# Kernel tuning notes

Measured on AMD Instinct MI355X. Metric: run time of the kernel, lower is better.

## Reference

```python
import jax, jax.numpy as jnp
import numpy as np

DIM_Q = 512
DIM_K = 512
DIM_V = 512
NUM_HEADS = 8
TEMPERATURE = 0.1
LN_EPS = 1e-5


def setup_inputs() -> dict:
    key = jax.random.key(0)
    ks = jax.random.split(key, 12)
    B, n_q, n_k = 8, 1024, 1024
    s = 0.02
    return {
        "Q": jax.random.normal(ks[0], (B, n_q, DIM_Q), jnp.float32),
        "K": jax.random.normal(ks[1], (B, n_k, DIM_K), jnp.float32),
        "mask": jnp.ones((B, n_k), dtype=bool),
        "Wq": jax.random.normal(ks[2], (DIM_Q, DIM_V), jnp.float32) * s,
        "bq": jnp.zeros((DIM_V,), jnp.float32),
        "Wk": jax.random.normal(ks[3], (DIM_K, DIM_V), jnp.float32) * s,
        "bk": jnp.zeros((DIM_V,), jnp.float32),
        "Wv": jax.random.normal(ks[4], (DIM_K, DIM_V), jnp.float32) * s,
        "bv": jnp.zeros((DIM_V,), jnp.float32),
        "Wo": jax.random.normal(ks[5], (DIM_V, DIM_V), jnp.float32) * s,
        "bo": jnp.zeros((DIM_V,), jnp.float32),
        "gamma": jnp.ones((DIM_V,), jnp.float32),
        "beta": jnp.zeros((DIM_V,), jnp.float32),
    }


def _mab(Q, K, mask, Wq, bq, Wk, bk, Wv, bv, Wo, bo, gamma, beta):
    B, n_q, _ = Q.shape
    n_k = K.shape[1]
    H = NUM_HEADS
    d_head = DIM_V // H
    # projections, split heads: [B, H, n, d_head]
    Qh = (Q @ Wq + bq).reshape(B, n_q, H, d_head).transpose(0, 2, 1, 3)
    Kh = (K @ Wk + bk).reshape(B, n_k, H, d_head).transpose(0, 2, 1, 3)
    Vh = (K @ Wv + bv).reshape(B, n_k, H, d_head).transpose(0, 2, 1, 3)
    scale = 1.0 / (np.sqrt(d_head) * TEMPERATURE)
    A = jnp.einsum("bhqd,bhkd->bhqk", Qh, Kh) * scale
    A = jnp.where(mask[:, None, None, :], A, -jnp.inf)
    A = jax.nn.softmax(A, axis=-1)
    O = jnp.einsum("bhqk,bhkd->bhqd", A, Vh)
    O = O.transpose(0, 2, 1, 3).reshape(B, n_q, DIM_V)
    # fused output FFN + residual + LN
    O = O + jax.nn.relu(O @ Wo + bo)
    mu = jnp.mean(O, axis=-1, keepdims=True)
    var = jnp.var(O, axis=-1, keepdims=True)
    return (O - mu) * jax.lax.rsqrt(var + LN_EPS) * gamma + beta


def reference(Q, K, mask, Wq, bq, Wk, bk, Wv, bv, Wo, bo, gamma, beta):
    return _mab(Q, K, mask, Wq, bq, Wk, bk, Wv, bv, Wo, bo, gamma, beta)
```

## Files before the change

kernel.cpp:

```cpp
#include <hip/hip_runtime.h>

typedef __bf16 bf16;
typedef bf16 bf16x4 __attribute__((ext_vector_type(4)));
typedef bf16 bf16x8 __attribute__((ext_vector_type(8)));
typedef float floatx4 __attribute__((ext_vector_type(4)));

#define NB 8
#define NQ 1024
#define NK 1024
#define DIM 512
#define NH 8
#define DH 64

__device__ __forceinline__ void async16(const void* g, void* l) {
    __builtin_amdgcn_global_load_lds(
        (const __attribute__((address_space(1))) unsigned int*)(unsigned long long)(g),
        (__attribute__((address_space(3))) unsigned int*)(unsigned long long)(l),
        16, 0, 0);
}

__global__ __launch_bounds__(256) void prep_fused(
    const float* __restrict__ Q, const float* __restrict__ K,
    const float* __restrict__ Wq, const float* __restrict__ Wk,
    const float* __restrict__ Wv, const float* __restrict__ Wo,
    bf16* __restrict__ Qb, bf16* __restrict__ Kb, bf16* __restrict__ Wt)
{
    __shared__ bf16 Tl[64][68];
    const int bid = blockIdx.x;
    if (bid < 4096) {
        const int i = bid * 256 + threadIdx.x;
        float4 a = ((const float4*)Q)[i];
        float4 c = ((const float4*)K)[i];
        bf16x4 qa = {(bf16)a.x, (bf16)a.y, (bf16)a.z, (bf16)a.w};
        bf16x4 ka = {(bf16)c.x, (bf16)c.y, (bf16)c.z, (bf16)c.w};
        *(bf16x4*)(Qb + (size_t)i * 4) = qa;
        *(bf16x4*)(Kb + (size_t)i * 4) = ka;
    } else {
        const int bid2 = bid - 4096;
        const int w = bid2 >> 6;
        const int bx = bid2 & 7, by = (bid2 >> 3) & 7;
        const float* W = (w == 0) ? Wq : (w == 1) ? Wk : (w == 2) ? Wv : Wo;
        bf16* out = Wt + (size_t)w * DIM * DIM;
        const int k0 = bx * 64, n0 = by * 64;
        const int tx = threadIdx.x & 15, ty = threadIdx.x >> 4;
        for (int pass = 0; pass < 4; ++pass) {
            int k = ty + pass * 16;
            float4 v = *(const float4*)&W[(size_t)(k0 + k) * DIM + n0 + tx * 4];
            Tl[tx * 4 + 0][k] = (bf16)v.x;
            Tl[tx * 4 + 1][k] = (bf16)v.y;
            Tl[tx * 4 + 2][k] = (bf16)v.z;
            Tl[tx * 4 + 3][k] = (bf16)v.w;
        }
        __syncthreads();
        for (int pass = 0; pass < 4; ++pass) {
            int n = ty + pass * 16;
            bf16x4 ov = *(const bf16x4*)&Tl[n][tx * 4];
            *(bf16x4*)&out[(size_t)(n0 + n) * DIM + k0 + tx * 4] = ov;
        }
    }
}

__global__ __launch_bounds__(256) void proj_fused(
    const bf16* __restrict__ Qb, const bf16* __restrict__ Kb,
    const bf16* __restrict__ Wt,
    const float* __restrict__ bq, const float* __restrict__ bk,
    const float* __restrict__ bv,
    bf16* __restrict__ Qp, bf16* __restrict__ Kp, bf16* __restrict__ Vpt)
{
    __shared__ __attribute__((aligned(16))) bf16 sh[24576];
    const int t = threadIdx.x;
    const int wave = t >> 6, lane = t & 63, quad = lane >> 4, l16 = lane & 15;
    const int wr = wave >> 1, wc = wave & 1;
    const int bid = blockIdx.x;
    const bool isQ = bid < 512;
    const bf16* A; const bf16* W; int m0, n0;
    if (isQ) { A = Qb; W = Wt;             m0 = (bid & 63) * 128;  n0 = (bid >> 6) * 64; }
    else     { int b2 = bid - 512;
               A = Kb; W = Wt + 512 * DIM; m0 = (b2 & 63) * 128;   n0 = (b2 >> 6) * 64; }

    const int r1 = t >> 3, s1 = t & 7;
    const int p1 = s1 ^ (r1 & 7);
    const bf16* aSrc = A + (size_t)(m0 + r1) * DIM + p1 * 8;
    const bf16* wSrc = W + (size_t)(n0 + r1) * DIM + p1 * 8;

    floatx4 acc[4][2];
    for (int i = 0; i < 4; ++i)
        for (int j = 0; j < 2; ++j) acc[i][j] = (floatx4){0.f, 0.f, 0.f, 0.f};

    #pragma unroll
    for (int j = 0; j < 4; ++j)
        async16(aSrc + (size_t)j * 32 * DIM, sh + (t + j * 256) * 8);
    #pragma unroll
    for (int j = 0; j < 2; ++j)
        async16(wSrc + (size_t)j * 32 * DIM, sh + 16384 + (t + j * 256) * 8);

    for (int kt = 0; kt < 8; ++kt) {
        __syncthreads();
        const int cur = kt & 1;
        bf16* Acur = sh + cur * 8192;
        bf16* Bcur = sh + 16384 + cur * 4096;
        if (kt < 7) {
            bf16* Anxt = sh + (1 - cur) * 8192;
            bf16* Bnxt = sh + 16384 + (1 - cur) * 4096;
            const int ko = (kt + 1) * 64;
            #pragma unroll
            for (int j = 0; j < 4; ++j)
                async16(aSrc + ko + (size_t)j * 32 * DIM, Anxt + (t + j * 256) * 8);
            #pragma unroll
            for (int j = 0; j < 2; ++j)
                async16(wSrc + ko + (size_t)j * 32 * DIM, Bnxt + (t + j * 256) * 8);
        }
        #pragma unroll
        for (int ks = 0; ks < 2; ++ks) {
            bf16x8 af[4], bfr[2];
            #pragma unroll
            for (int mi = 0; mi < 4; ++mi) {
                const int row = wr * 64 + mi * 16 + l16;
                af[mi] = *(const bf16x8*)(Acur + row * 64 + (((ks * 4 + quad) ^ (row & 7)) << 3));
            }
            #pragma unroll
            for (int ni = 0; ni < 2; ++ni) {
                const int row = wc * 32 + ni * 16 + l16;
                bfr[ni] = *(const bf16x8*)(Bcur + row * 64 + (((ks * 4 + quad) ^ (row & 7)) << 3));
            }
            #pragma unroll
            for (int mi = 0; mi < 4; ++mi)
                #pragma unroll
                for (int ni = 0; ni < 2; ++ni)
                    acc[mi][ni] = __builtin_amdgcn_mfma_f32_16x16x32_bf16(
                        af[mi], bfr[ni], acc[mi][ni], 0, 0, 0);
        }
    }

    const bool isV = (!isQ) && (n0 >= 512);
    if (!isV) {
        bf16* out = isQ ? Qp : Kp;
        const float* bias = isQ ? bq : bk;
        const float qscale = isQ ? 1.8033688f : 1.0f;
        for (int ni = 0; ni < 2; ++ni) {
            const int n = n0 + wc * 32 + ni * 16 + l16;
            const float bb = bias[n];
            const int hd = n >> 6, d = n & 63;
            for (int mi = 0; mi < 4; ++mi) {
                for (int r = 0; r < 4; ++r) {
                    const int m = m0 + wr * 64 + mi * 16 + quad * 4 + r;
                    const int b = m >> 10, q = m & 1023;
                    out[((size_t)(b * 8 + hd) * 1024 + q) * 64 + d] =
                        (bf16)((acc[mi][ni][r] + bb) * qscale);
                }
            }
        }
    } else {
        __syncthreads();
        for (int ni = 0; ni < 2; ++ni) {
            const int n = wc * 32 + ni * 16 + l16;
            const float bb = bv[n0 + n - 512];
            for (int mi = 0; mi < 4; ++mi) {
                const int mb = wr * 64 + mi * 16 + quad * 4;
                const int slot = ((mb >> 3) ^ (n & 15));
                bf16x4 pk = {(bf16)(acc[mi][ni][0] + bb), (bf16)(acc[mi][ni][1] + bb),
                             (bf16)(acc[mi][ni][2] + bb), (bf16)(acc[mi][ni][3] + bb)};
                *(bf16x4*)(sh + n * 128 + slot * 8 + (mb & 7)) = pk;
            }
        }
        __syncthreads();
        const int n = t >> 2, hf = t & 3;
        const int nv = n0 + n - 512, hd = nv >> 6, d = nv & 63;
        const int b = m0 >> 10, qb = m0 & 1023;
        bf16* dst = Vpt + ((size_t)(b * 8 + hd) * 64 + d) * 1024 + qb;
        #pragma unroll
        for (int j = 0; j < 4; ++j) {
            const int ch = hf * 4 + j;
            const int slot = ch ^ (n & 15);
            bf16x8 v8 = *(const bf16x8*)(sh + n * 128 + slot * 8);
            *(bf16x8*)(dst + ch * 8) = v8;
        }
    }
}

__global__ __launch_bounds__(256) void attn_kernel(
    const bf16* __restrict__ Qp, const bf16* __restrict__ Kp,
    const bf16* __restrict__ Vpt, const int* __restrict__ mask,
    bf16* __restrict__ Oa)
{
    const int bh = blockIdx.x & 63, qblk = blockIdx.x >> 6;
    const int b = bh >> 3, hd = bh & 7;
    const int t = threadIdx.x;
    const int wave = t >> 6, lane = t & 63, quad = lane >> 4, l16 = lane & 15;

    __shared__ __attribute__((aligned(16))) bf16 Kt[2][64 * 64];
    __shared__ __attribute__((aligned(16))) bf16 Vt[2][64 * 64];
    __shared__ __attribute__((aligned(16))) bf16 Pl[4][16 * 64];

    const bf16* Qbase = Qp + ((size_t)bh * NQ + qblk * 64 + wave * 16) * DH;
    const bf16* Kbase = Kp + (size_t)bh * NK * DH;
    const bf16* Vbase = Vpt + (size_t)bh * DH * NK;
    const int* mrow = mask + b * NK;

    bf16x8 qf[2];
    #pragma unroll
    for (int hh = 0; hh < 2; ++hh)
        qf[hh] = *(const bf16x8*)(Qbase + (size_t)l16 * DH + hh * 32 + quad * 8);

    bf16x8 onesv;
    #pragma unroll
    for (int j = 0; j < 8; ++j) onesv[j] = (bf16)1.0f;

    floatx4 o[4];
    floatx4 osum = (floatx4){0.f, 0.f, 0.f, 0.f};
    #pragma unroll
    for (int i = 0; i < 4; ++i) o[i] = (floatx4){0.f, 0.f, 0.f, 0.f};

    const int r1 = t >> 3, s1 = t & 7;
    const int p1 = s1 ^ (r1 & 7);
    const bf16* kSrc = Kbase + r1 * 64 + p1 * 8;
    const bf16* vSrc = Vbase + (size_t)r1 * 1024 + p1 * 8;

    async16(kSrc, Kt[0] + t * 8);
    async16(kSrc + 32 * 64, Kt[0] + (t + 256) * 8);
    async16(vSrc, Vt[0] + t * 8);
    async16(vSrc + (size_t)32 * 1024, Vt[0] + (t + 256) * 8);

    for (int kt = 0; kt < NK / 64; ++kt) {
        __syncthreads();
        const int cur = kt & 1;
        if (kt < NK / 64 - 1) {
            const int nxt = 1 - cur;
            async16(kSrc + (kt + 1) * 4096, Kt[nxt] + t * 8);
            async16(kSrc + (kt + 1) * 4096 + 32 * 64, Kt[nxt] + (t + 256) * 8);
            async16(vSrc + (kt + 1) * 64, Vt[nxt] + t * 8);
            async16(vSrc + (kt + 1) * 64 + (size_t)32 * 1024, Vt[nxt] + (t + 256) * 8);
        }

        bf16x8 kb[4][2];
        #pragma unroll
        for (int sub = 0; sub < 4; ++sub) {
            const int rowk = sub * 16 + l16;
            kb[sub][0] = *(const bf16x8*)(Kt[cur] + rowk * 64 + ((quad ^ (rowk & 7)) << 3));
            kb[sub][1] = *(const bf16x8*)(Kt[cur] + rowk * 64 + (((quad + 4) ^ (rowk & 7)) << 3));
        }
        floatx4 sf[4];
        __builtin_amdgcn_s_setprio(1);
        #pragma unroll
        for (int sub = 0; sub < 4; ++sub) {
            floatx4 s = {0.f, 0.f, 0.f, 0.f};
            s = __builtin_amdgcn_mfma_f32_16x16x32_bf16(kb[sub][0], qf[0], s, 0, 0, 0);
            s = __builtin_amdgcn_mfma_f32_16x16x32_bf16(kb[sub][1], qf[1], s, 0, 0, 0);
            sf[sub] = s;
        }
        __builtin_amdgcn_s_setprio(0);

        const int mv = mrow[kt * 64 + lane];
        if (!__all(mv != 0)) {
            #pragma unroll
            for (int sub = 0; sub < 4; ++sub) {
                const int4 m4 = *(const int4*)&mrow[kt * 64 + sub * 16 + quad * 4];
                if (!m4.x) sf[sub][0] = -3.0e38f;
                if (!m4.y) sf[sub][1] = -3.0e38f;
                if (!m4.z) sf[sub][2] = -3.0e38f;
                if (!m4.w) sf[sub][3] = -3.0e38f;
            }
        }
        #pragma unroll
        for (int sub = 0; sub < 4; ++sub) {
            sf[sub][0] = __builtin_amdgcn_exp2f(sf[sub][0]);
            sf[sub][1] = __builtin_amdgcn_exp2f(sf[sub][1]);
            sf[sub][2] = __builtin_amdgcn_exp2f(sf[sub][2]);
            sf[sub][3] = __builtin_amdgcn_exp2f(sf[sub][3]);
        }
        #pragma unroll
        for (int sub = 0; sub < 4; ++sub) {
            bf16x4 pk = {(bf16)sf[sub][0], (bf16)sf[sub][1],
                         (bf16)sf[sub][2], (bf16)sf[sub][3]};
            const int slot = (sub * 2 + (quad >> 1)) ^ (l16 & 7);
            *(bf16x4*)&Pl[wave][l16 * 64 + slot * 8 + (quad & 1) * 4] = pk;
        }
        bf16x8 af[2];
        #pragma unroll
        for (int hh = 0; hh < 2; ++hh) {
            const int slot = (hh * 4 + quad) ^ (l16 & 7);
            af[hh] = *(const bf16x8*)&Pl[wave][l16 * 64 + slot * 8];
        }
        __builtin_amdgcn_s_setprio(1);
        osum = __builtin_amdgcn_mfma_f32_16x16x32_bf16(af[0], onesv, osum, 0, 0, 0);
        osum = __builtin_amdgcn_mfma_f32_16x16x32_bf16(af[1], onesv, osum, 0, 0, 0);
        #pragma unroll
        for (int dsub = 0; dsub < 4; ++dsub) {
            const int rowd = dsub * 16 + l16;
            bf16x8 v0 = *(const bf16x8*)(Vt[cur] + rowd * 64 + ((quad ^ (rowd & 7)) << 3));
            bf16x8 v1 = *(const bf16x8*)(Vt[cur] + rowd * 64 + (((quad + 4) ^ (rowd & 7)) << 3));
            o[dsub] = __builtin_amdgcn_mfma_f32_16x16x32_bf16(af[0], v0, o[dsub], 0, 0, 0);
            o[dsub] = __builtin_amdgcn_mfma_f32_16x16x32_bf16(af[1], v1, o[dsub], 0, 0, 0);
        }
        __builtin_amdgcn_s_setprio(0);
    }

    float linv[4];
    #pragma unroll
    for (int r = 0; r < 4; ++r) linv[r] = 1.f / osum[r];
    for (int dsub = 0; dsub < 4; ++dsub) {
        for (int r = 0; r < 4; ++r) {
            const int q = qblk * 64 + wave * 16 + quad * 4 + r;
            const int col = hd * 64 + dsub * 16 + l16;
            Oa[((size_t)(b * NQ + q)) * DIM + col] = (bf16)(o[dsub][r] * linv[r]);
        }
    }
}

__global__ __launch_bounds__(256) void ffn_gemm(
    const bf16* __restrict__ Oa, const bf16* __restrict__ W,
    const float* __restrict__ bias, bf16* __restrict__ Yb)
{
    __shared__ __attribute__((aligned(16))) bf16 sh[32768];
    const int t = threadIdx.x;
    const int wave = t >> 6, lane = t & 63, quad = lane >> 4, l16 = lane & 15;
    const int wr = wave >> 1, wc = wave & 1;
    const int m0 = (blockIdx.x & 63) * 128, n0 = (blockIdx.x >> 6) * 64;
    const int ktr = n0 >> 6;

    const int r1 = t >> 3, s1 = t & 7;
    const int p1 = s1 ^ (r1 & 7);
    const bf16* aSrc = Oa + (size_t)(m0 + r1) * DIM + p1 * 8;
    const bf16* wSrc = W  + (size_t)(n0 + r1) * DIM + p1 * 8;

    floatx4 acc[4][2];
    for (int i = 0; i < 4; ++i)
        for (int j = 0; j < 2; ++j) acc[i][j] = (floatx4){0.f, 0.f, 0.f, 0.f};

    #pragma unroll
    for (int j = 0; j < 4; ++j)
        async16(aSrc + (size_t)j * 32 * DIM, sh + (t + j * 256) * 8);
    #pragma unroll
    for (int j = 0; j < 2; ++j)
        async16(wSrc + (size_t)j * 32 * DIM, sh + 16384 + (t + j * 256) * 8);

    for (int kt = 0; kt < 8; ++kt) {
        __syncthreads();
        const int cur = kt & 1;
        bf16* Acur = sh + cur * 8192;
        bf16* Bcur = sh + 16384 + cur * 4096;
        if (kt < 7) {
            bf16* Anxt = sh + (1 - cur) * 8192;
            bf16* Bnxt = sh + 16384 + (1 - cur) * 4096;
            const int ko = (kt + 1) * 64;
            #pragma unroll
            for (int j = 0; j < 4; ++j)
                async16(aSrc + ko + (size_t)j * 32 * DIM, Anxt + (t + j * 256) * 8);
            #pragma unroll
            for (int j = 0; j < 2; ++j)
                async16(wSrc + ko + (size_t)j * 32 * DIM, Bnxt + (t + j * 256) * 8);
        }
        if (kt == ktr) {
            #pragma unroll
            for (int j = 0; j < 4; ++j) {
                const int idx = t + j * 256;
                *(bf16x8*)(sh + 24576 + idx * 8) = *(const bf16x8*)(Acur + idx * 8);
            }
        }
        #pragma unroll
        for (int ks = 0; ks < 2; ++ks) {
            bf16x8 af[4], bfr[2];
            #pragma unroll
            for (int mi = 0; mi < 4; ++mi) {
                const int row = wr * 64 + mi * 16 + l16;
                af[mi] = *(const bf16x8*)(Acur + row * 64 + (((ks * 4 + quad) ^ (row & 7)) << 3));
            }
            #pragma unroll
            for (int ni = 0; ni < 2; ++ni) {
                const int row = wc * 32 + ni * 16 + l16;
                bfr[ni] = *(const bf16x8*)(Bcur + row * 64 + (((ks * 4 + quad) ^ (row & 7)) << 3));
            }
            #pragma unroll
            for (int mi = 0; mi < 4; ++mi)
                #pragma unroll
                for (int ni = 0; ni < 2; ++ni)
                    acc[mi][ni] = __builtin_amdgcn_mfma_f32_16x16x32_bf16(
                        af[mi], bfr[ni], acc[mi][ni], 0, 0, 0);
        }
    }
    __syncthreads();

    for (int ni = 0; ni < 2; ++ni) {
        const int n = n0 + wc * 32 + ni * 16 + l16;
        const int cl = wc * 32 + ni * 16 + l16;
        const int chi = cl >> 3, clo = cl & 7;
        const float bb = bias[n];
        for (int mi = 0; mi < 4; ++mi) {
            for (int r = 0; r < 4; ++r) {
                const int rl = wr * 64 + mi * 16 + quad * 4 + r;
                const float ov = (float)sh[24576 + rl * 64 + ((chi ^ (rl & 7)) << 3) + clo];
                Yb[(size_t)(m0 + rl) * DIM + n] = (bf16)(ov + fmaxf(acc[mi][ni][r] + bb, 0.f));
            }
        }
    }
}

__global__ __launch_bounds__(256) void ln_kernel(
    const bf16* __restrict__ Y, const float* __restrict__ gamma,
    const float* __restrict__ beta, float* __restrict__ out)
{
    const int row  = blockIdx.x * 4 + (threadIdx.x >> 6);
    const int lane = threadIdx.x & 63;
    bf16x8 v = *(const bf16x8*)(Y + (size_t)row * DIM + lane * 8);
    float f[8];
    float s = 0.f, sq = 0.f;
    #pragma unroll
    for (int j = 0; j < 8; ++j) {
        f[j] = (float)v[j];
        s += f[j];
        sq += f[j] * f[j];
    }
    for (int mk = 32; mk >= 1; mk >>= 1) {
        s  += __shfl_xor(s,  mk, 64);
        sq += __shfl_xor(sq, mk, 64);
    }
    const float mu  = s * (1.f / 512.f);
    const float var = sq * (1.f / 512.f) - mu * mu;
    const float inv = rsqrtf(var + 1e-5f);
    float4 g1 = ((const float4*)gamma)[lane * 2];
    float4 g2 = ((const float4*)gamma)[lane * 2 + 1];
    float4 b1 = ((const float4*)beta)[lane * 2];
    float4 b2 = ((const float4*)beta)[lane * 2 + 1];
    float4 o1, o2;
    o1.x = (f[0] - mu) * inv * g1.x + b1.x;
    o1.y = (f[1] - mu) * inv * g1.y + b1.y;
    o1.z = (f[2] - mu) * inv * g1.z + b1.z;
    o1.w = (f[3] - mu) * inv * g1.w + b1.w;
    o2.x = (f[4] - mu) * inv * g2.x + b2.x;
    o2.y = (f[5] - mu) * inv * g2.y + b2.y;
    o2.z = (f[6] - mu) * inv * g2.z + b2.z;
    o2.w = (f[7] - mu) * inv * g2.w + b2.w;
    float* orow = out + (size_t)row * DIM;
    ((float4*)orow)[lane * 2]     = o1;
    ((float4*)orow)[lane * 2 + 1] = o2;
}

extern "C" void kernel_launch(void* const* d_in, const int* in_sizes, int n_in,
                              void* d_out, int out_size, void* d_ws, size_t ws_size,
                              hipStream_t stream) {
    const float* Q  = (const float*)d_in[0];
    const float* K  = (const float*)d_in[1];
    const int*   mask = (const int*)d_in[2];
    const float* Wq = (const float*)d_in[3];
    const float* bq = (const float*)d_in[4];
    const float* Wk = (const float*)d_in[5];
    const float* bk = (const float*)d_in[6];
    const float* Wv = (const float*)d_in[7];
    const float* bv = (const float*)d_in[8];
    const float* Wo = (const float*)d_in[9];
    const float* bo = (const float*)d_in[10];
    const float* gamma = (const float*)d_in[11];
    const float* beta  = (const float*)d_in[12];

    char* ws = (char*)d_ws;
    bf16* Wt  = (bf16*)(ws);
    bf16* Qb  = (bf16*)(ws + 2097152);
    bf16* Kb  = (bf16*)(ws + 10485760);
    bf16* Qp  = (bf16*)(ws + 18874368);
    bf16* Kp  = (bf16*)(ws + 27262976);
    bf16* Vpt = (bf16*)(ws + 35651584);
    bf16* Oa  = (bf16*)(ws + 44040192);
    bf16* Yb  = (bf16*)(ws + 52428800);
    float* out = (float*)d_out;

    prep_fused<<<4352, 256, 0, stream>>>(Q, K, Wq, Wk, Wv, Wo, Qb, Kb, Wt);
    proj_fused<<<1536, 256, 0, stream>>>(Qb, Kb, Wt, bq, bk, bv, Qp, Kp, Vpt);
    attn_kernel<<<1024, 256, 0, stream>>>(Qp, Kp, Vpt, mask, Oa);
    ffn_gemm<<<512, 256, 0, stream>>>(Oa, Wt + 3 * 262144, bo, Yb);
    ln_kernel<<<2048, 256, 0, stream>>>(Yb, gamma, beta, out);
}
```

Measured before the change: 165.9 us.

## Split attention waves 2x2 over query and key halves with cross-wave reduction

Each wave now handles 32 query rows and half of each 64-key tile instead of 16 query rows and the full tile. K fragments are reused across two query groups and each V fragment is loaded once for two MFMAs, which cuts LDS reads per MFMA. At the end, partner waves exchange partial O accumulators and row sums through shared memory and each wave writes half of the results. It also adds an occupancy hint to launch bounds and a smaller P scratch layout with a new swizzle, at the cost of an extra reduction phase and more accumulator registers.

New measurement: 189.4 us. 1.14x slower.

```diff
diff --git a/kernel.cpp b/kernel.cpp
--- a/kernel.cpp
+++ b/kernel.cpp
@@ -178,7 +178,7 @@
     }
 }
 
-__global__ __launch_bounds__(256) void attn_kernel(
+__global__ __launch_bounds__(256, 4) void attn_kernel(
     const bf16* __restrict__ Qp, const bf16* __restrict__ Kp,
     const bf16* __restrict__ Vpt, const int* __restrict__ mask,
     bf16* __restrict__ Oa)
@@ -187,29 +187,36 @@
     const int b = bh >> 3, hd = bh & 7;
     const int t = threadIdx.x;
     const int wave = t >> 6, lane = t & 63, quad = lane >> 4, l16 = lane & 15;
+    const int wq = wave >> 1, wk = wave & 1;
 
     __shared__ __attribute__((aligned(16))) bf16 Kt[2][64 * 64];
     __shared__ __attribute__((aligned(16))) bf16 Vt[2][64 * 64];
-    __shared__ __attribute__((aligned(16))) bf16 Pl[4][16 * 64];
-
-    const bf16* Qbase = Qp + ((size_t)bh * NQ + qblk * 64 + wave * 16) * DH;
+    __shared__ __attribute__((aligned(16))) bf16 Pl[4][32 * 32];
+
+    const bf16* Qbase = Qp + ((size_t)bh * NQ + qblk * 64 + wq * 32) * DH;
     const bf16* Kbase = Kp + (size_t)bh * NK * DH;
     const bf16* Vbase = Vpt + (size_t)bh * DH * NK;
     const int* mrow = mask + b * NK;
 
-    bf16x8 qf[2];
-    #pragma unroll
-    for (int hh = 0; hh < 2; ++hh)
-        qf[hh] = *(const bf16x8*)(Qbase + (size_t)l16 * DH + hh * 32 + quad * 8);
+    bf16x8 qf[2][2];
+    #pragma unroll
+    for (int qg = 0; qg < 2; ++qg)
+        #pragma unroll
+        for (int hh = 0; hh < 2; ++hh)
+            qf[qg][hh] = *(const bf16x8*)(Qbase + (size_t)(qg * 16 + l16) * DH + hh * 32 + quad * 8);
 
     bf16x8 onesv;
     #pragma unroll
     for (int j = 0; j < 8; ++j) onesv[j] = (bf16)1.0f;
 
-    floatx4 o[4];
-    floatx4 osum = (floatx4){0.f, 0.f, 0.f, 0.f};
-    #pragma unroll
-    for (int i = 0; i < 4; ++i) o[i] = (floatx4){0.f, 0.f, 0.f, 0.f};
+    floatx4 o[2][4];
+    floatx4 osum[2];
+    #pragma unroll
+    for (int qg = 0; qg < 2; ++qg) {
+        osum[qg] = (floatx4){0.f, 0.f, 0.f, 0.f};
+        #pragma unroll
+        for (int i = 0; i < 4; ++i) o[qg][i] = (floatx4){0.f, 0.f, 0.f, 0.f};
+    }
 
     const int r1 = t >> 3, s1 = t & 7;
     const int p1 = s1 ^ (r1 & 7);
@@ -220,6 +227,8 @@
     async16(kSrc + 32 * 64, Kt[0] + (t + 256) * 8);
     async16(vSrc, Vt[0] + t * 8);
     async16(vSrc + (size_t)32 * 1024, Vt[0] + (t + 256) * 8);
+
+    const int xor3 = (l16 & 3) ^ ((l16 >> 2) & 3);
 
     for (int kt = 0; kt < NK / 64; ++kt) {
         __syncthreads();
@@ -232,77 +241,101 @@
             async16(vSrc + (kt + 1) * 64 + (size_t)32 * 1024, Vt[nxt] + (t + 256) * 8);
         }
 
-        bf16x8 kb[4][2];
-        #pragma unroll
-        for (int sub = 0; sub < 4; ++sub) {
-            const int rowk = sub * 16 + l16;
+        bf16x8 kb[2][2];
+        #pragma unroll
+        for (int sub = 0; sub < 2; ++sub) {
+            const int rowk = wk * 32 + sub * 16 + l16;
             kb[sub][0] = *(const bf16x8*)(Kt[cur] + rowk * 64 + ((quad ^ (rowk & 7)) << 3));
             kb[sub][1] = *(const bf16x8*)(Kt[cur] + rowk * 64 + (((quad + 4) ^ (rowk & 7)) << 3));
         }
-        floatx4 sf[4];
+        floatx4 sf[2][2];
         __builtin_amdgcn_s_setprio(1);
         #pragma unroll
-        for (int sub = 0; sub < 4; ++sub) {
-            floatx4 s = {0.f, 0.f, 0.f, 0.f};
-            s = __builtin_amdgcn_mfma_f32_16x16x32_bf16(kb[sub][0], qf[0], s, 0, 0, 0);
-            s = __builtin_amdgcn_mfma_f32_16x16x32_bf16(kb[sub][1], qf[1], s, 0, 0, 0);
-            sf[sub] = s;
-        }
+        for (int sub = 0; sub < 2; ++sub)
+            #pragma unroll
+            for (int qg = 0; qg < 2; ++qg) {
+                floatx4 s = {0.f, 0.f, 0.f, 0.f};
+                s = __builtin_amdgcn_mfma_f32_16x16x32_bf16(kb[sub][0], qf[qg][0], s, 0, 0, 0);
+                s = __builtin_amdgcn_mfma_f32_16x16x32_bf16(kb[sub][1], qf[qg][1], s, 0, 0, 0);
+                sf[sub][qg] = s;
+            }
         __builtin_amdgcn_s_setprio(0);
 
         const int mv = mrow[kt * 64 + lane];
         if (!__all(mv != 0)) {
             #pragma unroll
-            for (int sub = 0; sub < 4; ++sub) {
-                const int4 m4 = *(const int4*)&mrow[kt * 64 + sub * 16 + quad * 4];
-                if (!m4.x) sf[sub][0] = -3.0e38f;
-                if (!m4.y) sf[sub][1] = -3.0e38f;
-                if (!m4.z) sf[sub][2] = -3.0e38f;
-                if (!m4.w) sf[sub][3] = -3.0e38f;
-            }
-        }
-        #pragma unroll
-        for (int sub = 0; sub < 4; ++sub) {
-            sf[sub][0] = __builtin_amdgcn_exp2f(sf[sub][0]);
-            sf[sub][1] = __builtin_amdgcn_exp2f(sf[sub][1]);
-            sf[sub][2] = __builtin_amdgcn_exp2f(sf[sub][2]);
-            sf[sub][3] = __builtin_amdgcn_exp2f(sf[sub][3]);
-        }
-        #pragma unroll
-        for (int sub = 0; sub < 4; ++sub) {
-            bf16x4 pk = {(bf16)sf[sub][0], (bf16)sf[sub][1],
-                         (bf16)sf[sub][2], (bf16)sf[sub][3]};
-            const int slot = (sub * 2 + (quad >> 1)) ^ (l16 & 7);
-            *(bf16x4*)&Pl[wave][l16 * 64 + slot * 8 + (quad & 1) * 4] = pk;
-        }
+            for (int sub = 0; sub < 2; ++sub) {
+                const int4 m4 = *(const int4*)&mrow[kt * 64 + wk * 32 + sub * 16 + quad * 4];
+                #pragma unroll
+                for (int qg = 0; qg < 2; ++qg) {
+                    if (!m4.x) sf[sub][qg][0] = -3.0e38f;
+                    if (!m4.y) sf[sub][qg][1] = -3.0e38f;
+                    if (!m4.z) sf[sub][qg][2] = -3.0e38f;
+                    if (!m4.w) sf[sub][qg][3] = -3.0e38f;
+                }
+            }
+        }
+        #pragma unroll
+        for (int sub = 0; sub < 2; ++sub)
+            #pragma unroll
+            for (int qg = 0; qg < 2; ++qg) {
+                bf16x4 pk = {(bf16)__builtin_amdgcn_exp2f(sf[sub][qg][0]),
+                             (bf16)__builtin_amdgcn_exp2f(sf[sub][qg][1]),
+                             (bf16)__builtin_amdgcn_exp2f(sf[sub][qg][2]),
+                             (bf16)__builtin_amdgcn_exp2f(sf[sub][qg][3])};
+                const int slot = (sub * 2 + (quad >> 1)) ^ xor3;
+                *(bf16x4*)&Pl[wave][(qg * 16 + l16) * 32 + slot * 8 + (quad & 1) * 4] = pk;
+            }
         bf16x8 af[2];
         #pragma unroll
-        for (int hh = 0; hh < 2; ++hh) {
-            const int slot = (hh * 4 + quad) ^ (l16 & 7);
-            af[hh] = *(const bf16x8*)&Pl[wave][l16 * 64 + slot * 8];
-        }
+        for (int qg = 0; qg < 2; ++qg)
+            af[qg] = *(const bf16x8*)&Pl[wave][(qg * 16 + l16) * 32 + ((quad ^ xor3) << 3)];
+
         __builtin_amdgcn_s_setprio(1);
-        osum = __builtin_amdgcn_mfma_f32_16x16x32_bf16(af[0], onesv, osum, 0, 0, 0);
-        osum = __builtin_amdgcn_mfma_f32_16x16x32_bf16(af[1], onesv, osum, 0, 0, 0);
+        osum[0] = __builtin_amdgcn_mfma_f32_16x16x32_bf16(af[0], onesv, osum[0], 0, 0, 0);
+        osum[1] = __builtin_amdgcn_mfma_f32_16x16x32_bf16(af[1], onesv, osum[1], 0, 0, 0);
         #pragma unroll
         for (int dsub = 0; dsub < 4; ++dsub) {
-            const int rowd = dsub * 16 + l16;
-            bf16x8 v0 = *(const bf16x8*)(Vt[cur] + rowd * 64 + ((quad ^ (rowd & 7)) << 3));
-            bf16x8 v1 = *(const bf16x8*)(Vt[cur] + rowd * 64 + (((quad + 4) ^ (rowd & 7)) << 3));
-            o[dsub] = __builtin_amdgcn_mfma_f32_16x16x32_bf16(af[0], v0, o[dsub], 0, 0, 0);
-            o[dsub] = __builtin_amdgcn_mfma_f32_16x16x32_bf16(af[1], v1, o[dsub], 0, 0, 0);
+            const int d = dsub * 16 + l16;
+            bf16x8 vb = *(const bf16x8*)(Vt[cur] + d * 64 + (((wk * 4 + quad) ^ (d & 7)) << 3));
+            o[0][dsub] = __builtin_amdgcn_mfma_f32_16x16x32_bf16(af[0], vb, o[0][dsub], 0, 0, 0);
+            o[1][dsub] = __builtin_amdgcn_mfma_f32_16x16x32_bf16(af[1], vb, o[1][dsub], 0, 0, 0);
         }
         __builtin_amdgcn_s_setprio(0);
     }
 
-    float linv[4];
-    #pragma unroll
-    for (int r = 0; r < 4; ++r) linv[r] = 1.f / osum[r];
-    for (int dsub = 0; dsub < 4; ++dsub) {
-        for (int r = 0; r < 4; ++r) {
-            const int q = qblk * 64 + wave * 16 + quad * 4 + r;
-            const int col = hd * 64 + dsub * 16 + l16;
-            Oa[((size_t)(b * NQ + q)) * DIM + col] = (bf16)(o[dsub][r] * linv[r]);
+    __syncthreads();
+    float* scr  = (float*)Kt;
+    float* scrL = (float*)Vt;
+
+    {
+        float* reg = scr + wave * 1024;
+        #pragma unroll
+        for (int dsub = 0; dsub < 4; ++dsub)
+            *(floatx4*)(reg + dsub * 256 + lane * 4) = o[1 - wk][dsub];
+        if (l16 == 0) {
+            #pragma unroll
+            for (int r = 0; r < 4; ++r)
+                scrL[wave * 16 + quad * 4 + r] = osum[1 - wk][r];
+        }
+    }
+    __syncthreads();
+    {
+        const int partner = wq * 2 + (1 - wk);
+        float* reg = scr + partner * 1024;
+        #pragma unroll
+        for (int dsub = 0; dsub < 4; ++dsub)
+            o[wk][dsub] += *(const floatx4*)(reg + dsub * 256 + lane * 4);
+        float linv[4];
+        #pragma unroll
+        for (int r = 0; r < 4; ++r)
+            linv[r] = 1.f / (osum[wk][r] + scrL[partner * 16 + quad * 4 + r]);
+        for (int dsub = 0; dsub < 4; ++dsub) {
+            for (int r = 0; r < 4; ++r) {
+                const int q = qblk * 64 + wq * 32 + wk * 16 + quad * 4 + r;
+                const int col = hd * 64 + dsub * 16 + l16;
+                Oa[((size_t)(b * NQ + q)) * DIM + col] = (bf16)(o[wk][dsub][r] * linv[r]);
+            }
         }
     }
 }
```
